# Optimization experiments

Measured on AMD Instinct MI355X. Metric: run time of the kernel, lower is better.

## Reference

```python
import jax, jax.numpy as jnp
import numpy as np
from jax import lax

N_CLASSES = 10
N_EXPERTS = 45  # 10 choose 2
EPS = 1e-5

# lookup table: (i1, i2) with i1 < i2 -> flat expert id (matches nested loop order)
_tbl = np.zeros((N_CLASSES, N_CLASSES), dtype=np.int32)
_k = 0
for _i1 in range(N_CLASSES):
    for _i2 in range(_i1 + 1, N_CLASSES):
        _tbl[_i1, _i2] = _k
        _k += 1
PAIR_TABLE = jnp.asarray(_tbl)


def _downscale(x):
    # AvgPool2d(3, stride=3) on 28x28 -> 9x9 (floor: uses top-left 27x27)
    B = x.shape[0]
    return x[:, :, :27, :27].reshape(B, 1, 9, 3, 9, 3).mean(axis=(3, 5))


def _bn_eval(h, gamma, beta, mean, var):
    scale = gamma * lax.rsqrt(var + EPS)
    return h * scale[None, :, None, None] + (beta - mean * scale)[None, :, None, None]


def _stage1(x, w1, b1, g1, be1, m1, v1, fcw1, fcb1):
    xd = _downscale(x)                                         # [B,1,9,9]
    h = lax.conv_general_dilated(xd, w1, (1, 1), 'VALID',
                                 dimension_numbers=('NCHW', 'OIHW', 'NCHW'))
    h = h + b1[None, :, None, None]                            # [B,20,7,7]
    h = _bn_eval(h, g1, be1, m1, v1)
    h = jax.nn.relu(h)
    B = h.shape[0]
    h = h[:, :, :6, :6].reshape(B, 20, 3, 2, 3, 2).max(axis=(3, 5))  # maxpool2 -> [B,20,3,3]
    h = h.reshape(B, 180)
    return h @ fcw1.T + fcb1                                   # [B,10] raw logits


def reference(x, w1, b1, g1, be1, m1, v1, fcw1, fcb1,
              w2, b2, g2, be2, m2, v2, fcw2, fcb2):
    B = x.shape[0]
    logits1 = _stage1(x, w1, b1, g1, be1, m1, v1, fcw1, fcb1)  # [B,10]
    ls1 = jax.nn.log_softmax(logits1, axis=1)

    # routing: top-2 class indices, sorted ascending, -> pairwise expert id
    top2 = jnp.sort(jnp.argsort(ls1, axis=1)[:, -2:], axis=1)  # [B,2]
    idx0, idx1 = top2[:, 0], top2[:, 1]
    eid = PAIR_TABLE[idx0, idx1]                               # [B]

    # stage 2 (TinyNet2) with per-example gathered expert params
    xd = _downscale(x)                                         # [B,1,9,9]
    # extract 5x5 conv patches (valid, stride 1): output spatial 5x5
    patches = jnp.stack([xd[:, 0, i:i + 5, j:j + 5]
                         for i in range(5) for j in range(5)], axis=1)  # [B,25,5,5]
    Wsel = w2.reshape(N_EXPERTS, 15, 25)[eid]                  # [B,15,25]
    h = jnp.einsum('bkhw,bok->bohw', patches, Wsel) + b2[eid][:, :, None, None]  # [B,15,5,5]
    scale = (g2 * lax.rsqrt(v2 + EPS))[eid]                    # [B,15]
    shift = (be2 - m2 * g2 * lax.rsqrt(v2 + EPS))[eid]
    h = h * scale[:, :, None, None] + shift[:, :, None, None]
    h = jax.nn.relu(h)
    h = h[:, :, :4, :4].reshape(B, 15, 2, 2, 2, 2).max(axis=(3, 5))  # [B,15,2,2]
    feat = h.reshape(B, 60)
    s2 = jnp.einsum('bf,bof->bo', feat, fcw2[eid]) + fcb2[eid]  # [B,2]

    # combine: scatter the two expert logits into the routed columns
    rows = jnp.arange(B)
    out = jnp.full((B, N_CLASSES), -100.0, dtype=logits1.dtype)
    out = out.at[rows, idx0].set(s2[:, 0]).at[rows, idx1].set(s2[:, 1])
    # eval-mode bypass: use stage1 raw logits if max log-prob > 0.3
    use1 = jnp.max(ls1, axis=1) > 0.3
    out = jnp.where(use1[:, None], logits1, out)
    out = jax.nn.log_softmax(out, axis=1)
    return (logits1, out)


def setup_inputs() -> dict:
    key = jax.random.key(0)
    ks = jax.random.split(key, 18)
    B = 65536
    s = 0.1
    return {
        'x': jax.random.normal(ks[0], (B, 1, 28, 28), dtype=jnp.float32),
        # stage1 (TinyNet, 20 kernels, k=3)
        'w1': jax.random.normal(ks[1], (20, 1, 3, 3), dtype=jnp.float32) * s,
        'b1': jax.random.normal(ks[2], (20,), dtype=jnp.float32) * s,
        'g1': jax.random.normal(ks[3], (20,), dtype=jnp.float32) * s + 1.0,
        'be1': jax.random.normal(ks[4], (20,), dtype=jnp.float32) * s,
        'm1': jax.random.normal(ks[5], (20,), dtype=jnp.float32) * s,
        'v1': jax.random.uniform(ks[6], (20,), dtype=jnp.float32) + 0.5,
        'fcw1': jax.random.normal(ks[7], (10, 180), dtype=jnp.float32) * s,
        'fcb1': jax.random.normal(ks[8], (10,), dtype=jnp.float32) * s,
        # 45 stacked stage2 experts (TinyNet2, 15 kernels, k=5)
        'w2': jax.random.normal(ks[9], (45, 15, 1, 5, 5), dtype=jnp.float32) * s,
        'b2': jax.random.normal(ks[10], (45, 15), dtype=jnp.float32) * s,
        'g2': jax.random.normal(ks[11], (45, 15), dtype=jnp.float32) * s + 1.0,
        'be2': jax.random.normal(ks[12], (45, 15), dtype=jnp.float32) * s,
        'm2': jax.random.normal(ks[13], (45, 15), dtype=jnp.float32) * s,
        'v2': jax.random.uniform(ks[14], (45, 15), dtype=jnp.float32) + 0.5,
        'fcw2': jax.random.normal(ks[15], (45, 2, 60), dtype=jnp.float32) * s,
        'fcb2': jax.random.normal(ks[16], (45, 2), dtype=jnp.float32) * s,
    }
```

## Files before the change

kernel.cpp:

```cpp
#include <hip/hip_runtime.h>
#include <cmath>

#define EPSF 1e-5f


__global__ __launch_bounds__(256) void setup_tables(
    const float* __restrict__ w1, const float* __restrict__ b1,
    const float* __restrict__ g1, const float* __restrict__ be1,
    const float* __restrict__ m1, const float* __restrict__ v1,
    const float* __restrict__ w2, const float* __restrict__ b2,
    const float* __restrict__ g2, const float* __restrict__ be2,
    const float* __restrict__ m2, const float* __restrict__ v2,
    const float* __restrict__ fcw2, const float* __restrict__ fcb2,
    float* __restrict__ ws, int B)
{
  const int t  = blockIdx.x * blockDim.x + threadIdx.x;
  const int nt = gridDim.x * blockDim.x;
  float* W2F  = ws + (size_t)81 * B;
  float* B2F  = W2F + 20160;
  float* FC2  = W2F + 20880;
  float* FCB2 = W2F + 26640;
  float* W1F  = W2F + 26730;
  float* B1F  = W2F + 26910;

  for (int idx = t; idx < 20160; idx += nt) {
    int kk = idx & 3, rest = idx >> 2;
    int e = rest % 45, ok4 = rest / 45;
    int k4 = ok4 % 7, o = ok4 / 7;
    int k = k4 * 4 + kk;
    float val = 0.0f;
    if (o < 15 && k < 25) {
      float s = g2[e*15+o] / sqrtf(v2[e*15+o] + EPSF);
      val = w2[(e*15+o)*25 + k] * s;
    }
    W2F[idx] = val;
  }
  for (int idx = t; idx < 720; idx += nt) {
    int e = idx % 45, o = idx / 45;
    float val = 0.0f;
    if (o < 15) {
      float s = g2[e*15+o] / sqrtf(v2[e*15+o] + EPSF);
      val = b2[e*15+o]*s + be2[e*15+o] - m2[e*15+o]*s;
    }
    B2F[idx] = val;
  }
  for (int idx = t; idx < 5760; idx += nt) {
    int kk = idx & 3, rest = idx >> 2;
    int e = rest % 45, t2 = rest / 45;
    int o = t2 % 16, oo = t2 / 16;
    FC2[idx] = (o < 15) ? fcw2[(e*2+oo)*60 + o*4 + kk] : 0.0f;
  }
  for (int idx = t; idx < 90; idx += nt) {
    int e = idx % 45, oo = idx / 45;
    FCB2[idx] = fcb2[e*2+oo];
  }
  for (int idx = t; idx < 180; idx += nt) {
    int ch = idx / 9;
    float s = g1[ch] / sqrtf(v1[ch] + EPSF);
    W1F[idx] = w1[idx] * s;
  }
  for (int idx = t; idx < 20; idx += nt) {
    float s = g1[idx] / sqrtf(v1[idx] + EPSF);
    B1F[idx] = b1[idx]*s + be1[idx] - m1[idx]*s;
  }
}

__global__ __launch_bounds__(256) void downscale_t(
    const float* __restrict__ x, float* __restrict__ ws, int B)
{
  __shared__ float sxd[64 * 81];
  const int tid = threadIdx.x;
  const int b0  = blockIdx.x * 64;

  #pragma unroll 1
  for (int idx = tid; idx < 1728; idx += 256) {
    int s = idx / 27, j = idx % 27;
    int r = j / 3, trip = j % 3;
    const float* xb = x + (size_t)(b0 + s) * 784;
    float s0 = 0.f, s1 = 0.f, s2 = 0.f;
    #pragma unroll
    for (int dr = 0; dr < 3; dr++) {
      const float* row = xb + (3*r + dr) * 28;
      const float4* rv = reinterpret_cast<const float4*>(row) + 2*trip;
      float4 A = rv[0], Bv = rv[1], Cv = rv[2];
      if (trip == 0)      { s0 += A.x+A.y+A.z;  s1 += A.w+Bv.x+Bv.y;  s2 += Bv.z+Bv.w+Cv.x; }
      else if (trip == 1) { s0 += A.y+A.z+A.w;  s1 += Bv.x+Bv.y+Bv.z; s2 += Bv.w+Cv.x+Cv.y; }
      else                { s0 += A.z+A.w+Bv.x; s1 += Bv.y+Bv.z+Bv.w; s2 += Cv.x+Cv.y+Cv.z; }
    }
    float* q = &sxd[s*81 + r*9 + 3*trip];
    q[0] = s0 * (1.0f/9.0f); q[1] = s1 * (1.0f/9.0f); q[2] = s2 * (1.0f/9.0f);
  }
  __syncthreads();

  #pragma unroll 1
  for (int idx = tid; idx < 5184; idx += 256) {
    int k = idx >> 6, s = idx & 63;
    ws[(size_t)k * B + (b0 + s)] = sxd[s*81 + k];
  }
}

__global__ __launch_bounds__(256, 2) void main_dual(
    const float* __restrict__ ws,
    const float* __restrict__ fcw1, const float* __restrict__ fcb1,
    float* __restrict__ out, int B)
{
  const int g   = blockIdx.x * 256 + threadIdx.x;
  const int b   = g >> 1;
  const int sub = g & 1;

  const float* W2F  = ws + (size_t)81 * B;
  const float* B2F  = W2F + 20160;
  const float* FC2  = W2F + 20880;
  const float* FCB2 = W2F + 26640;
  const float* W1F  = W2F + 26730;
  const float* B1F  = W2F + 26910;

  float xd[81];
  {
    const float* p = ws + b;
    #pragma unroll
    for (int k = 0; k < 81; k++) xd[k] = p[(size_t)k * B];
  }

  float P[10], Q[10];
  #pragma unroll
  for (int c = 0; c < 10; c++) { P[c] = 0.0f; Q[c] = 0.0f; }

  #pragma unroll 1
  for (int s1 = 0; s1 < 10; s1++) {
    const int ch = 2*s1 + sub;
    float w[9];
    #pragma unroll
    for (int k = 0; k < 9; k++) w[k] = W1F[ch*9 + k];
    float bb = B1F[ch];
    float feat[9];
    #pragma unroll
    for (int pr = 0; pr < 3; pr++) {
      #pragma unroll
      for (int pc = 0; pc < 3; pc++) {
        float c00 = bb, c01 = bb, c10 = bb, c11 = bb;
        #pragma unroll
        for (int dr = 0; dr < 3; dr++) {
          #pragma unroll
          for (int dc = 0; dc < 3; dc++) {
            float wk = w[dr*3 + dc];
            c00 = fmaf(xd[(2*pr+0+dr)*9 + 2*pc+0+dc], wk, c00);
            c01 = fmaf(xd[(2*pr+0+dr)*9 + 2*pc+1+dc], wk, c01);
            c10 = fmaf(xd[(2*pr+1+dr)*9 + 2*pc+0+dc], wk, c10);
            c11 = fmaf(xd[(2*pr+1+dr)*9 + 2*pc+1+dc], wk, c11);
          }
        }
        feat[pr*3+pc] = fmaxf(fmaxf(fmaxf(c00, c01), fmaxf(c10, c11)), 0.0f);
      }
    }
    #pragma unroll
    for (int c = 0; c < 10; c++) {
      float accP = P[c], accQ = Q[c];
      #pragma unroll
      for (int pp = 0; pp < 9; pp++) {
        accP = fmaf(feat[pp], fcw1[c*180 + (2*s1+0)*9 + pp], accP);
        accQ = fmaf(feat[pp], fcw1[c*180 + (2*s1+1)*9 + pp], accQ);
      }
      P[c] = accP; Q[c] = accQ;
    }
  }

  float logits[10];
  #pragma unroll
  for (int c = 0; c < 10; c++) {
    float sel = sub ? Q[c] : P[c];
    logits[c] = sel + __shfl_xor(sel, 1) + fcb1[c];
  }

  int i1 = 0; float v1m = logits[0];
  #pragma unroll
  for (int c = 1; c < 10; c++) { if (logits[c] >= v1m) { v1m = logits[c]; i1 = c; } }
  int i2 = 0; float v2m = -3.0e38f;
  #pragma unroll
  for (int c = 0; c < 10; c++) { if (c != i1 && logits[c] >= v2m) { v2m = logits[c]; i2 = c; } }
  int idx0 = i1 < i2 ? i1 : i2;
  int idx1 = i1 < i2 ? i2 : i1;
  int eid  = 8*idx0 - (idx0*(idx0-1))/2 + idx1 - 1;

  float mx = v1m;
  float sume = 0.0f;
  #pragma unroll
  for (int c = 0; c < 10; c++) sume += expf(logits[c] - mx);
  bool use1 = (-logf(sume)) > 0.3f;

  const float4* W2F4 = reinterpret_cast<const float4*>(W2F);
  const float4* FC24 = reinterpret_cast<const float4*>(FC2);

  float s2a = 0.0f, s2b = 0.0f;
  float4 wv[7], fa, fb; float bias;
  {
    const int o = sub;
    #pragma unroll
    for (int k4 = 0; k4 < 7; k4++) wv[k4] = W2F4[(o*7 + k4)*45 + eid];
    bias = B2F[o*45 + eid];
    fa = FC24[(0*16 + o)*45 + eid];
    fb = FC24[(1*16 + o)*45 + eid];
  }

  #pragma unroll 1
  for (int j = 0; j < 8; j++) {
    float4 nwv[7], nfa, nfb; float nbias;
    if (j < 7) {
      const int o = 2*(j+1) + sub;
      #pragma unroll
      for (int k4 = 0; k4 < 7; k4++) nwv[k4] = W2F4[(o*7 + k4)*45 + eid];
      nbias = B2F[o*45 + eid];
      nfa = FC24[(0*16 + o)*45 + eid];
      nfb = FC24[(1*16 + o)*45 + eid];
    }
    float feats[4];
    #pragma unroll
    for (int ph = 0; ph < 2; ph++) {
      #pragma unroll
      for (int pw = 0; pw < 2; pw++) {
        float c00 = bias, c01 = bias, c10 = bias, c11 = bias;
        #pragma unroll
        for (int i = 0; i < 5; i++) {
          #pragma unroll
          for (int jj = 0; jj < 5; jj++) {
            int k = i*5 + jj;
            float wk = (k%4==0) ? wv[k/4].x : (k%4==1) ? wv[k/4].y :
                       (k%4==2) ? wv[k/4].z : wv[k/4].w;
            c00 = fmaf(xd[(2*ph+0+i)*9 + 2*pw+0+jj], wk, c00);
            c01 = fmaf(xd[(2*ph+0+i)*9 + 2*pw+1+jj], wk, c01);
            c10 = fmaf(xd[(2*ph+1+i)*9 + 2*pw+0+jj], wk, c10);
            c11 = fmaf(xd[(2*ph+1+i)*9 + 2*pw+1+jj], wk, c11);
          }
        }
        feats[ph*2+pw] = fmaxf(fmaxf(fmaxf(c00, c01), fmaxf(c10, c11)), 0.0f);
      }
    }
    s2a = fmaf(feats[0], fa.x, fmaf(feats[1], fa.y, fmaf(feats[2], fa.z, fmaf(feats[3], fa.w, s2a))));
    s2b = fmaf(feats[0], fb.x, fmaf(feats[1], fb.y, fmaf(feats[2], fb.z, fmaf(feats[3], fb.w, s2b))));
    if (j < 7) {
      #pragma unroll
      for (int k4 = 0; k4 < 7; k4++) wv[k4] = nwv[k4];
      bias = nbias; fa = nfa; fb = nfb;
    }
  }
  s2a += __shfl_xor(s2a, 1);
  s2b += __shfl_xor(s2b, 1);
  s2a += FCB2[eid];
  s2b += FCB2[45 + eid];

  float o10[10];
  #pragma unroll
  for (int c = 0; c < 10; c++) {
    float v = -100.0f;
    v = (c == idx0) ? s2a : v;
    v = (c == idx1) ? s2b : v;
    o10[c] = use1 ? logits[c] : v;
  }
  float m2x = o10[0];
  #pragma unroll
  for (int c = 1; c < 10; c++) m2x = fmaxf(m2x, o10[c]);
  float se2 = 0.0f;
  #pragma unroll
  for (int c = 0; c < 10; c++) se2 += expf(o10[c] - m2x);
  float lse2 = m2x + logf(se2);

  size_t base = (size_t)b * 10;
  if (sub == 0) {
    #pragma unroll
    for (int c = 0; c < 10; c++) out[base + c] = logits[c];
  } else {
    #pragma unroll
    for (int c = 0; c < 10; c++) out[(size_t)B*10 + base + c] = o10[c] - lse2;
  }
}

extern "C" void kernel_launch(void* const* d_in, const int* in_sizes, int n_in,
                              void* d_out, int out_size, void* d_ws, size_t ws_size,
                              hipStream_t stream) {
  const float* x    = (const float*)d_in[0];
  const float* w1   = (const float*)d_in[1];
  const float* b1   = (const float*)d_in[2];
  const float* g1   = (const float*)d_in[3];
  const float* be1  = (const float*)d_in[4];
  const float* m1   = (const float*)d_in[5];
  const float* v1   = (const float*)d_in[6];
  const float* fcw1 = (const float*)d_in[7];
  const float* fcb1 = (const float*)d_in[8];
  const float* w2   = (const float*)d_in[9];
  const float* b2   = (const float*)d_in[10];
  const float* g2   = (const float*)d_in[11];
  const float* be2  = (const float*)d_in[12];
  const float* m2   = (const float*)d_in[13];
  const float* v2   = (const float*)d_in[14];
  const float* fcw2 = (const float*)d_in[15];
  const float* fcb2 = (const float*)d_in[16];
  float* out = (float*)d_out;
  float* ws  = (float*)d_ws;
  const int B = in_sizes[0] / 784;

  setup_tables<<<80, 256, 0, stream>>>(w1, b1, g1, be1, m1, v1,
                                       w2, b2, g2, be2, m2, v2, fcw2, fcb2, ws, B);
  downscale_t<<<B/64, 256, 0, stream>>>(x, ws, B);
  main_dual<<<(2*B)/256, 256, 0, stream>>>(ws, fcw1, fcb1, out, B);
}
```

Measured before the change: 387.3 us.

## Fuse downscale into main kernel via shared memory, drop transposed workspace

Merges the separate downscale kernel into the main kernel. Each block now downsamples 128 samples into shared memory, and each thread pair reads its 81 pooled values from LDS instead of from a transposed global workspace. This removes one kernel launch and the global write/read round trip of the pooled images. In exchange it uses about 41KB of LDS per block, which may limit occupancy alongside the two-blocks launch bound. The LDS reads also have a stride of 81 floats per sample, which may cause bank conflicts.

```diff
diff --git a/kernel.cpp b/kernel.cpp
--- a/kernel.cpp
+++ b/kernel.cpp
@@ -12,16 +12,16 @@
     const float* __restrict__ g2, const float* __restrict__ be2,
     const float* __restrict__ m2, const float* __restrict__ v2,
     const float* __restrict__ fcw2, const float* __restrict__ fcb2,
-    float* __restrict__ ws, int B)
+    float* __restrict__ ws)
 {
   const int t  = blockIdx.x * blockDim.x + threadIdx.x;
   const int nt = gridDim.x * blockDim.x;
-  float* W2F  = ws + (size_t)81 * B;
-  float* B2F  = W2F + 20160;
-  float* FC2  = W2F + 20880;
-  float* FCB2 = W2F + 26640;
-  float* W1F  = W2F + 26730;
-  float* B1F  = W2F + 26910;
+  float* W2F  = ws;
+  float* B2F  = ws + 20160;
+  float* FC2  = ws + 20880;
+  float* FCB2 = ws + 26640;
+  float* W1F  = ws + 26730;
+  float* B1F  = ws + 26910;
 
   for (int idx = t; idx < 20160; idx += nt) {
     int kk = idx & 3, rest = idx >> 2;
@@ -65,61 +65,56 @@
   }
 }
 
-__global__ __launch_bounds__(256) void downscale_t(
-    const float* __restrict__ x, float* __restrict__ ws, int B)
-{
-  __shared__ float sxd[64 * 81];
-  const int tid = threadIdx.x;
-  const int b0  = blockIdx.x * 64;
-
-  #pragma unroll 1
-  for (int idx = tid; idx < 1728; idx += 256) {
-    int s = idx / 27, j = idx % 27;
-    int r = j / 3, trip = j % 3;
-    const float* xb = x + (size_t)(b0 + s) * 784;
-    float s0 = 0.f, s1 = 0.f, s2 = 0.f;
-    #pragma unroll
-    for (int dr = 0; dr < 3; dr++) {
-      const float* row = xb + (3*r + dr) * 28;
-      const float4* rv = reinterpret_cast<const float4*>(row) + 2*trip;
-      float4 A = rv[0], Bv = rv[1], Cv = rv[2];
-      if (trip == 0)      { s0 += A.x+A.y+A.z;  s1 += A.w+Bv.x+Bv.y;  s2 += Bv.z+Bv.w+Cv.x; }
-      else if (trip == 1) { s0 += A.y+A.z+A.w;  s1 += Bv.x+Bv.y+Bv.z; s2 += Bv.w+Cv.x+Cv.y; }
-      else                { s0 += A.z+A.w+Bv.x; s1 += Bv.y+Bv.z+Bv.w; s2 += Cv.x+Cv.y+Cv.z; }
-    }
-    float* q = &sxd[s*81 + r*9 + 3*trip];
-    q[0] = s0 * (1.0f/9.0f); q[1] = s1 * (1.0f/9.0f); q[2] = s2 * (1.0f/9.0f);
-  }
-  __syncthreads();
-
-  #pragma unroll 1
-  for (int idx = tid; idx < 5184; idx += 256) {
-    int k = idx >> 6, s = idx & 63;
-    ws[(size_t)k * B + (b0 + s)] = sxd[s*81 + k];
-  }
-}
-
-__global__ __launch_bounds__(256, 2) void main_dual(
+__global__ __launch_bounds__(256, 2) void fused2(
+    const float* __restrict__ x,
     const float* __restrict__ ws,
     const float* __restrict__ fcw1, const float* __restrict__ fcb1,
     float* __restrict__ out, int B)
 {
-  const int g   = blockIdx.x * 256 + threadIdx.x;
-  const int b   = g >> 1;
-  const int sub = g & 1;
-
-  const float* W2F  = ws + (size_t)81 * B;
-  const float* B2F  = W2F + 20160;
-  const float* FC2  = W2F + 20880;
-  const float* FCB2 = W2F + 26640;
-  const float* W1F  = W2F + 26730;
-  const float* B1F  = W2F + 26910;
+  __shared__ float sxd[128 * 81];
+  const int tid = threadIdx.x;
+  const int b0  = blockIdx.x * 128;
+  const int nvalid = (B - b0 < 128) ? (B - b0) : 128;
+
+  #pragma unroll 1
+  for (int idx = tid; idx < 3456; idx += 256) {
+    int s = idx / 27, j = idx % 27;
+    if (s < nvalid) {
+      int r = j / 3, trip = j % 3;
+      const float* xb = x + (size_t)(b0 + s) * 784;
+      float s0 = 0.f, s1 = 0.f, s2 = 0.f;
+      #pragma unroll
+      for (int dr = 0; dr < 3; dr++) {
+        const float* row = xb + (3*r + dr) * 28;
+        const float4* rv = reinterpret_cast<const float4*>(row) + 2*trip;
+        float4 A = rv[0], Bv = rv[1], Cv = rv[2];
+        if (trip == 0)      { s0 += A.x+A.y+A.z;  s1 += A.w+Bv.x+Bv.y;  s2 += Bv.z+Bv.w+Cv.x; }
+        else if (trip == 1) { s0 += A.y+A.z+A.w;  s1 += Bv.x+Bv.y+Bv.z; s2 += Bv.w+Cv.x+Cv.y; }
+        else                { s0 += A.z+A.w+Bv.x; s1 += Bv.y+Bv.z+Bv.w; s2 += Cv.x+Cv.y+Cv.z; }
+      }
+      float* q = &sxd[s*81 + r*9 + 3*trip];
+      q[0] = s0 * (1.0f/9.0f); q[1] = s1 * (1.0f/9.0f); q[2] = s2 * (1.0f/9.0f);
+    }
+  }
+  __syncthreads();
+
+  const int s_local = tid >> 1;
+  const int sub     = tid & 1;
+  const int b       = b0 + s_local;
+  if (s_local >= nvalid) return;
+
+  const float* W2F  = ws;
+  const float* B2F  = ws + 20160;
+  const float* FC2  = ws + 20880;
+  const float* FCB2 = ws + 26640;
+  const float* W1F  = ws + 26730;
+  const float* B1F  = ws + 26910;
 
   float xd[81];
   {
-    const float* p = ws + b;
-    #pragma unroll
-    for (int k = 0; k < 81; k++) xd[k] = p[(size_t)k * B];
+    const float* p = &sxd[s_local * 81];
+    #pragma unroll
+    for (int k = 0; k < 81; k++) xd[k] = p[k];
   }
 
   float P[10], Q[10];
@@ -299,7 +294,6 @@
   const int B = in_sizes[0] / 784;
 
   setup_tables<<<80, 256, 0, stream>>>(w1, b1, g1, be1, m1, v1,
-                                       w2, b2, g2, be2, m2, v2, fcw2, fcb2, ws, B);
-  downscale_t<<<B/64, 256, 0, stream>>>(x, ws, B);
-  main_dual<<<(2*B)/256, 256, 0, stream>>>(ws, fcw1, fcb1, out, B);
+                                       w2, b2, g2, be2, m2, v2, fcw2, fcb2, ws);
+  fused2<<<(B + 127)/128, 256, 0, stream>>>(x, ws, fcw1, fcb1, out, B);
 }
```

New measurement: 369.9 us. 4.5% less time.
